# Optimization experiments

Measured on AMD Instinct MI355X. Metric: run time of the kernel, lower is better.

## Reference

```python
import jax, jax.numpy as jnp
import numpy as np

SCALE_VALUE = 1  # init kwarg; divide scores by sqrt(scale_value)


def setup_inputs() -> dict:
    key = jax.random.key(0)
    k1, k2 = jax.random.split(key)
    B, S, D = 8, 4096, 128
    inputs = jax.random.normal(k1, (B, S, D), dtype=jnp.float32)
    kernel = jax.random.normal(k2, (3, D, D), dtype=jnp.float32) * 0.05
    return {"inputs": inputs, "kernel": kernel}


def reference(inputs, kernel):
    # Q/K/V projections: [B,S,D] @ [D,D]
    wq = jnp.einsum('bsd,de->bse', inputs, kernel[0])
    wk = jnp.einsum('bsd,de->bse', inputs, kernel[1])
    wv = jnp.einsum('bsd,de->bse', inputs, kernel[2])
    # full attention score matrix [B,S,S], scaled by 1/sqrt(scale_value)
    qk = jnp.einsum('bqd,bkd->bqk', wq, wk) / (SCALE_VALUE ** 0.5)
    attn = jax.nn.softmax(qk, axis=-1)
    v = jnp.einsum('bqk,bkd->bqd', attn, wv)
    # mean pool over sequence -> [B,D]
    return jnp.mean(v, axis=1)
```

## Files before the change

kernel.cpp:

```cpp
#include <hip/hip_runtime.h>

#define Bsz 8
#define Ssz 4096
#define Dsz 128

typedef short bf16x8 __attribute__((ext_vector_type(8)));
typedef float f32x4 __attribute__((ext_vector_type(4)));
typedef float f32x16 __attribute__((ext_vector_type(16)));
typedef int i32x2 __attribute__((ext_vector_type(2)));
typedef int i32x4 __attribute__((ext_vector_type(4)));
typedef unsigned int u32;

union B8 { u32 u[4]; bf16x8 v; };

__device__ __forceinline__ u32 pkbf(float a, float b) {
  u32 ra = __float_as_uint(a) + 0x8000u;
  u32 rb = __float_as_uint(b) + 0x8000u;
  return __builtin_amdgcn_perm(rb, ra, 0x07060302u);
}
__device__ __forceinline__ short f2bf(float f) {
  u32 r = __float_as_uint(f) + 0x8000u;
  return (short)(r >> 16);
}

__device__ __forceinline__ void gll16(const void* g, void* l) {
  __builtin_amdgcn_global_load_lds((const __attribute__((address_space(1))) void*)g,
                                   (__attribute__((address_space(3))) void*)l, 16, 0, 0);
}


__global__ __launch_bounds__(256, 2) void proj_kernel(
    const float* __restrict__ x, const float* __restrict__ wsrc,
    short* __restrict__ Qs, short* __restrict__ Ks, short* __restrict__ Vp) {
  __shared__ short xb[64 * 136];
  __shared__ short ob[8192];

  const int rb = blockIdx.x;
  const int t = threadIdx.x;
  const int wv = t >> 6, lane = t & 63, l31 = lane & 31, h = lane >> 5;

  {
    const float* xsrc = x + (size_t)rb * 64 * Dsz;
    #pragma unroll
    for (int p = 0; p < 8; ++p) {
      int idx4 = p * 256 + t;
      int row = idx4 >> 5;
      int c4 = (idx4 & 31) << 2;
      f32x4 v = *(const f32x4*)&xsrc[idx4 * 4];
      i32x2 pr;
      pr[0] = pkbf(v[0], v[1]);
      pr[1] = pkbf(v[2], v[3]);
      *(i32x2*)&xb[row * 136 + c4] = pr;
    }
  }
  __syncthreads();

  bf16x8 xf[2][8];
  #pragma unroll
  for (int st = 0; st < 2; ++st)
    #pragma unroll
    for (int c = 0; c < 8; ++c)
      xf[st][c] = *(const bf16x8*)&xb[(st * 32 + l31) * 136 + c * 16 + 8 * h];

  for (int mat = 0; mat < 3; ++mat) {
    const float* wm = wsrc + (size_t)mat * Dsz * Dsz;
    const float scale = (mat == 0) ? 1.44269504088896340736f : 1.0f;
    bf16x8 wf[8];
    #pragma unroll
    for (int c = 0; c < 8; ++c) {
      const float* p = wm + (size_t)(c * 16 + 8 * h) * Dsz + wv * 32 + l31;
      B8 tmp;
      #pragma unroll
      for (int j = 0; j < 4; ++j)
        tmp.u[j] = pkbf(p[(2 * j) * Dsz] * scale, p[(2 * j + 1) * Dsz] * scale);
      wf[c] = tmp.v;
    }

    if (mat < 2) {
      #pragma unroll
      for (int st = 0; st < 2; ++st) {
        f32x16 acc = {};
        #pragma unroll
        for (int c = 0; c < 8; ++c)
          acc = __builtin_amdgcn_mfma_f32_32x32x16_bf16(wf[c], xf[st][c], acc, 0, 0, 0);
        if (st == 0) __syncthreads();
        #pragma unroll
        for (int g = 0; g < 4; ++g) {
          int e0 = wv * 32 + 8 * g + 4 * h;
          int s = st * 32 + l31;
          i32x2 pr;
          pr[0] = pkbf(acc[4 * g + 0], acc[4 * g + 1]);
          pr[1] = pkbf(acc[4 * g + 2], acc[4 * g + 3]);
          *(i32x2*)&ob[(e0 >> 3) * 512 + s * 8 + (e0 & 7)] = pr;
        }
      }
    } else {
      #pragma unroll
      for (int st = 0; st < 2; ++st) {
        f32x16 acc = {};
        #pragma unroll
        for (int c = 0; c < 8; ++c)
          acc = __builtin_amdgcn_mfma_f32_32x32x16_bf16(xf[st][c], wf[c], acc, 0, 0, 0);
        if (st == 0) __syncthreads();
        int e = wv * 32 + l31;
        #pragma unroll
        for (int r = 0; r < 16; ++r) {
          int s = st * 32 + (r & 3) + 8 * (r >> 2) + 4 * h;
          ob[s * 128 + e] = f2bf(acc[r]);
        }
      }
    }
    __syncthreads();
    short* dst = (mat == 0 ? Qs : mat == 1 ? Ks : Vp) + (size_t)rb * 8192;
    #pragma unroll
    for (int p = 0; p < 4; ++p)
      *(i32x4*)&dst[(p * 256 + t) * 8] = *(const i32x4*)&ob[(p * 256 + t) * 8];
  }
}

__global__ __launch_bounds__(256, 2) void lsum_kernel(
    const short* __restrict__ Qs, const short* __restrict__ Ks,
    float* __restrict__ lpart) {
  __shared__ short kbuf[2][16384];

  const int b = blockIdx.x, qt = blockIdx.y, kt = blockIdx.z;
  const int t = threadIdx.x;
  const int wv = t >> 6, lane = t & 63, l31 = lane & 31, h = lane >> 5;

  bf16x8 qf[2][8];
  {
    const short* qsrc = Qs + (size_t)(b * 64 + qt * 4 + wv) * 8192;
    #pragma unroll
    for (int nq = 0; nq < 2; ++nq)
      #pragma unroll
      for (int c = 0; c < 8; ++c)
        qf[nq][c] = *(const bf16x8*)&qsrc[(2 * c + h) * 512 + (nq * 32 + l31) * 8];
  }
  float rs2[2] = {0.f, 0.f};

  const char* kbase = (const char*)(Ks + (size_t)(b * 64 + kt * 16) * 8192);
  #define STAGE_K2(it_, bf_)                                                    \
    { const char* src_ = kbase + (size_t)(it_) * 32768;                         \
      _Pragma("unroll")                                                         \
      for (int i_ = 0; i_ < 8; ++i_) {                                          \
        int p_ = wv * 8 + i_;                                                   \
        gll16(src_ + p_ * 1024 + lane * 16, (char*)kbuf[bf_] + p_ * 1024);      \
      } }

  STAGE_K2(0, 0);
  __syncthreads();

  for (int it = 0; it < 8; ++it) {
    const int cur = it & 1;
    if (it < 7) STAGE_K2(it + 1, cur ^ 1);
    #pragma unroll
    for (int mk = 0; mk < 4; ++mk) {
      bf16x8 kf[8];
      #pragma unroll
      for (int c = 0; c < 8; ++c)
        kf[c] = *(const bf16x8*)&kbuf[cur][(mk >> 1) * 8192 + (2 * c + h) * 512 +
                                           ((mk & 1) * 32 + l31) * 8];
      f32x16 s0 = {}, s1 = {};
      #pragma unroll
      for (int c = 0; c < 8; ++c) {
        s0 = __builtin_amdgcn_mfma_f32_32x32x16_bf16(kf[c], qf[0][c], s0, 0, 0, 0);
        s1 = __builtin_amdgcn_mfma_f32_32x32x16_bf16(kf[c], qf[1][c], s1, 0, 0, 0);
      }
      #pragma unroll
      for (int r = 0; r < 16; ++r) rs2[0] += __builtin_amdgcn_exp2f(s0[r]);
      #pragma unroll
      for (int r = 0; r < 16; ++r) rs2[1] += __builtin_amdgcn_exp2f(s1[r]);
    }
    __syncthreads();
  }

  #pragma unroll
  for (int nq = 0; nq < 2; ++nq) {
    float v = rs2[nq] + __shfl_xor(rs2[nq], 32, 64);
    if (h == 0)
      lpart[((size_t)kt * 8 + b) * 4096 + qt * 256 + wv * 64 + nq * 32 + l31] = v;
  }
}

__global__ __launch_bounds__(256, 2) void attnv_kernel(
    const short* __restrict__ Qs, const short* __restrict__ Ks,
    const float* __restrict__ lpart, float* __restrict__ gpart) {
  __shared__ short kbuf[2][8192];
  __shared__ float linv_lds[256];
  __shared__ float gw[4][1024];

  const int b = blockIdx.x, qt = blockIdx.y, kt = blockIdx.z;
  const int t = threadIdx.x;
  const int wv = t >> 6, lane = t & 63, l31 = lane & 31, h = lane >> 5;

  {
    int q = qt * 256 + t;
    float l = 0.f;
    #pragma unroll
    for (int k2 = 0; k2 < 4; ++k2) l += lpart[((size_t)k2 * 8 + b) * 4096 + q];
    linv_lds[t] = 1.f / (l * (float)Ssz);
  }

  bf16x8 qf[2][8];
  {
    const short* qsrc = Qs + (size_t)(b * 64 + qt * 4 + wv) * 8192;
    #pragma unroll
    for (int mq = 0; mq < 2; ++mq)
      #pragma unroll
      for (int c = 0; c < 8; ++c)
        qf[mq][c] = *(const bf16x8*)&qsrc[(2 * c + h) * 512 + (mq * 32 + l31) * 8];
  }
  __syncthreads();

  float li[2][16];
  #pragma unroll
  for (int mq = 0; mq < 2; ++mq)
    #pragma unroll
    for (int r = 0; r < 16; ++r)
      li[mq][r] = linv_lds[wv * 64 + mq * 32 + (r & 3) + 8 * (r >> 2) + 4 * h];

  const char* kbase = (const char*)(Ks + (size_t)(b * 64 + kt * 16) * 8192);
  #define STAGE_K1(it_, bf_)                                                    \
    { const char* src_ = kbase + (size_t)(it_) * 16384;                         \
      _Pragma("unroll")                                                         \
      for (int i_ = 0; i_ < 4; ++i_) {                                          \
        int p_ = wv * 4 + i_;                                                   \
        gll16(src_ + p_ * 1024 + lane * 16, (char*)kbuf[bf_] + p_ * 1024);      \
      } }

  STAGE_K1(0, 0);
  __syncthreads();

  for (int it = 0; it < 16; ++it) {
    const int cur = it & 1;
    if (it < 15) STAGE_K1(it + 1, cur ^ 1);
    #pragma unroll
    for (int nk = 0; nk < 2; ++nk) {
      bf16x8 kf[8];
      #pragma unroll
      for (int c = 0; c < 8; ++c)
        kf[c] = *(const bf16x8*)&kbuf[cur][(2 * c + h) * 512 + (nk * 32 + l31) * 8];
      f32x16 s0 = {}, s1 = {};
      #pragma unroll
      for (int c = 0; c < 8; ++c) {
        s0 = __builtin_amdgcn_mfma_f32_32x32x16_bf16(qf[0][c], kf[c], s0, 0, 0, 0);
        s1 = __builtin_amdgcn_mfma_f32_32x32x16_bf16(qf[1][c], kf[c], s1, 0, 0, 0);
      }
      float gp = 0.f;
      #pragma unroll
      for (int r = 0; r < 16; ++r)
        gp += li[0][r] * __builtin_amdgcn_exp2f(s0[r]) +
              li[1][r] * __builtin_amdgcn_exp2f(s1[r]);
      gp += __shfl_xor(gp, 32, 64);
      if (h == 0) gw[wv][it * 64 + nk * 32 + l31] = gp;
    }
    __syncthreads();
  }

  float* gdst = gpart + (((size_t)(b * 16 + qt) * 4) + kt) * 1024;
  #pragma unroll
  for (int j = 0; j < 4; ++j) {
    int idx = j * 256 + t;
    gdst[idx] = (gw[0][idx] + gw[1][idx]) + (gw[2][idx] + gw[3][idx]);
  }
}

__global__ __launch_bounds__(256) void gemv_kernel(
    const float* __restrict__ gpart, const short* __restrict__ Vp,
    float* __restrict__ out) {
  __shared__ float Gs[128];
  __shared__ float pwb[512];
  const int b = blockIdx.x, ks = blockIdx.y;
  const int t = threadIdx.x;
  if (t < 128) {
    int k = ks * 128 + t;
    int kt = k >> 10, kl = k & 1023;
    float s = 0.f;
    #pragma unroll
    for (int qt = 0; qt < 16; ++qt)
      s += gpart[(((size_t)(b * 16 + qt) * 4) + kt) * 1024 + kl];
    Gs[t] = s;
  }
  __syncthreads();
  const int dp = t & 63, kq = t >> 6;
  const short* vr = Vp + ((size_t)b * 4096 + ks * 128 + kq * 32) * 128 + 2 * dp;
  float a0 = 0.f, a1 = 0.f;
  #pragma unroll 8
  for (int k = 0; k < 32; ++k) {
    u32 pair = *(const u32*)&vr[(size_t)k * 128];
    float g = Gs[kq * 32 + k];
    a0 += g * __uint_as_float(pair << 16);
    a1 += g * __uint_as_float(pair & 0xffff0000u);
  }
  pwb[kq * 128 + 2 * dp] = a0;
  pwb[kq * 128 + 2 * dp + 1] = a1;
  __syncthreads();
  if (t < 128) {
    float s = (pwb[t] + pwb[128 + t]) + (pwb[256 + t] + pwb[384 + t]);
    atomicAdd(&out[b * 128 + t], s);
  }
}

extern "C" void kernel_launch(void* const* d_in, const int* in_sizes, int n_in,
                              void* d_out, int out_size, void* d_ws, size_t ws_size,
                              hipStream_t stream) {
  const float* x = (const float*)d_in[0];
  const float* w = (const float*)d_in[1];
  short* Qs = (short*)d_ws;
  short* Ks = Qs + (size_t)Bsz * Ssz * Dsz;
  short* Vp = Ks + (size_t)Bsz * Ssz * Dsz;
  float* lpart = (float*)(Vp + (size_t)Bsz * Ssz * Dsz);
  float* gpart = lpart + 4 * Bsz * Ssz;

  hipMemsetAsync(d_out, 0, Bsz * Dsz * sizeof(float), stream);
  proj_kernel<<<dim3(Bsz * Ssz / 64), dim3(256), 0, stream>>>(x, w, Qs, Ks, Vp);
  lsum_kernel<<<dim3(Bsz, 16, 4), dim3(256), 0, stream>>>(Qs, Ks, lpart);
  attnv_kernel<<<dim3(Bsz, 16, 4), dim3(256), 0, stream>>>(Qs, Ks, lpart, gpart);
  gemv_kernel<<<dim3(Bsz, 32), dim3(256), 0, stream>>>(gpart, Vp, (float*)d_out);
}
```

Baseline: 144.3 us.

## Widen attention blocks to 512 threads, fold normalization into MFMA accumulator, drop memset

```diff
diff --git a/kernel.cpp b/kernel.cpp
--- a/kernel.cpp
+++ b/kernel.cpp
@@ -31,13 +31,16 @@
 
 __global__ __launch_bounds__(256, 2) void proj_kernel(
     const float* __restrict__ x, const float* __restrict__ wsrc,
-    short* __restrict__ Qs, short* __restrict__ Ks, short* __restrict__ Vp) {
+    short* __restrict__ Qs, short* __restrict__ Ks, short* __restrict__ Vp,
+    float* __restrict__ out0) {
   __shared__ short xb[64 * 136];
   __shared__ short ob[8192];
 
   const int rb = blockIdx.x;
   const int t = threadIdx.x;
   const int wv = t >> 6, lane = t & 63, l31 = lane & 31, h = lane >> 5;
+
+  if (rb < 4) out0[rb * 256 + t] = 0.f;
 
   {
     const float* xsrc = x + (size_t)rb * 64 * Dsz;
@@ -118,7 +121,7 @@
   }
 }
 
-__global__ __launch_bounds__(256, 2) void lsum_kernel(
+__global__ __launch_bounds__(512, 4) void lsum_kernel(
     const short* __restrict__ Qs, const short* __restrict__ Ks,
     float* __restrict__ lpart) {
   __shared__ short kbuf[2][16384];
@@ -129,7 +132,7 @@
 
   bf16x8 qf[2][8];
   {
-    const short* qsrc = Qs + (size_t)(b * 64 + qt * 4 + wv) * 8192;
+    const short* qsrc = Qs + (size_t)(b * 64 + qt * 8 + wv) * 8192;
     #pragma unroll
     for (int nq = 0; nq < 2; ++nq)
       #pragma unroll
@@ -138,131 +141,120 @@
   }
   float rs2[2] = {0.f, 0.f};
 
-  const char* kbase = (const char*)(Ks + (size_t)(b * 64 + kt * 16) * 8192);
-  #define STAGE_K2(it_, bf_)                                                    \
+  const char* kbase = (const char*)(Ks + (size_t)(b * 64 + kt * 8) * 8192);
+  #define STAGE2(it_, bf_)                                                      \
     { const char* src_ = kbase + (size_t)(it_) * 32768;                         \
-      _Pragma("unroll")                                                         \
-      for (int i_ = 0; i_ < 8; ++i_) {                                          \
-        int p_ = wv * 8 + i_;                                                   \
-        gll16(src_ + p_ * 1024 + lane * 16, (char*)kbuf[bf_] + p_ * 1024);      \
-      } }
-
-  STAGE_K2(0, 0);
-  __syncthreads();
-
-  for (int it = 0; it < 8; ++it) {
-    const int cur = it & 1;
-    if (it < 7) STAGE_K2(it + 1, cur ^ 1);
-    #pragma unroll
-    for (int mk = 0; mk < 4; ++mk) {
-      bf16x8 kf[8];
-      #pragma unroll
-      for (int c = 0; c < 8; ++c)
-        kf[c] = *(const bf16x8*)&kbuf[cur][(mk >> 1) * 8192 + (2 * c + h) * 512 +
-                                           ((mk & 1) * 32 + l31) * 8];
-      f32x16 s0 = {}, s1 = {};
-      #pragma unroll
-      for (int c = 0; c < 8; ++c) {
-        s0 = __builtin_amdgcn_mfma_f32_32x32x16_bf16(kf[c], qf[0][c], s0, 0, 0, 0);
-        s1 = __builtin_amdgcn_mfma_f32_32x32x16_bf16(kf[c], qf[1][c], s1, 0, 0, 0);
-      }
-      #pragma unroll
-      for (int r = 0; r < 16; ++r) rs2[0] += __builtin_amdgcn_exp2f(s0[r]);
-      #pragma unroll
-      for (int r = 0; r < 16; ++r) rs2[1] += __builtin_amdgcn_exp2f(s1[r]);
-    }
-    __syncthreads();
-  }
-
-  #pragma unroll
-  for (int nq = 0; nq < 2; ++nq) {
-    float v = rs2[nq] + __shfl_xor(rs2[nq], 32, 64);
-    if (h == 0)
-      lpart[((size_t)kt * 8 + b) * 4096 + qt * 256 + wv * 64 + nq * 32 + l31] = v;
-  }
-}
-
-__global__ __launch_bounds__(256, 2) void attnv_kernel(
-    const short* __restrict__ Qs, const short* __restrict__ Ks,
-    const float* __restrict__ lpart, float* __restrict__ gpart) {
-  __shared__ short kbuf[2][8192];
-  __shared__ float linv_lds[256];
-  __shared__ float gw[4][1024];
-
-  const int b = blockIdx.x, qt = blockIdx.y, kt = blockIdx.z;
-  const int t = threadIdx.x;
-  const int wv = t >> 6, lane = t & 63, l31 = lane & 31, h = lane >> 5;
-
-  {
-    int q = qt * 256 + t;
-    float l = 0.f;
-    #pragma unroll
-    for (int k2 = 0; k2 < 4; ++k2) l += lpart[((size_t)k2 * 8 + b) * 4096 + q];
-    linv_lds[t] = 1.f / (l * (float)Ssz);
-  }
-
-  bf16x8 qf[2][8];
-  {
-    const short* qsrc = Qs + (size_t)(b * 64 + qt * 4 + wv) * 8192;
-    #pragma unroll
-    for (int mq = 0; mq < 2; ++mq)
-      #pragma unroll
-      for (int c = 0; c < 8; ++c)
-        qf[mq][c] = *(const bf16x8*)&qsrc[(2 * c + h) * 512 + (mq * 32 + l31) * 8];
-  }
-  __syncthreads();
-
-  float li[2][16];
-  #pragma unroll
-  for (int mq = 0; mq < 2; ++mq)
-    #pragma unroll
-    for (int r = 0; r < 16; ++r)
-      li[mq][r] = linv_lds[wv * 64 + mq * 32 + (r & 3) + 8 * (r >> 2) + 4 * h];
-
-  const char* kbase = (const char*)(Ks + (size_t)(b * 64 + kt * 16) * 8192);
-  #define STAGE_K1(it_, bf_)                                                    \
-    { const char* src_ = kbase + (size_t)(it_) * 16384;                         \
       _Pragma("unroll")                                                         \
       for (int i_ = 0; i_ < 4; ++i_) {                                          \
         int p_ = wv * 4 + i_;                                                   \
         gll16(src_ + p_ * 1024 + lane * 16, (char*)kbuf[bf_] + p_ * 1024);      \
       } }
 
-  STAGE_K1(0, 0);
-  __syncthreads();
-
-  for (int it = 0; it < 16; ++it) {
+  STAGE2(0, 0);
+  __syncthreads();
+
+  for (int it = 0; it < 4; ++it) {
     const int cur = it & 1;
-    if (it < 15) STAGE_K1(it + 1, cur ^ 1);
+    if (it < 3) STAGE2(it + 1, cur ^ 1);
+    #pragma unroll
+    for (int mk = 0; mk < 4; ++mk) {
+      const int kb0 = (mk >> 1) * 8192 + ((mk & 1) * 32 + l31) * 8;
+      f32x16 s0 = {}, s1 = {};
+      #pragma unroll
+      for (int c = 0; c < 8; ++c) {
+        bf16x8 kf = *(const bf16x8*)&kbuf[cur][kb0 + (2 * c + h) * 512];
+        s0 = __builtin_amdgcn_mfma_f32_32x32x16_bf16(kf, qf[0][c], s0, 0, 0, 0);
+        s1 = __builtin_amdgcn_mfma_f32_32x32x16_bf16(kf, qf[1][c], s1, 0, 0, 0);
+      }
+      #pragma unroll
+      for (int r = 0; r < 16; ++r) rs2[0] += __builtin_amdgcn_exp2f(s0[r]);
+      #pragma unroll
+      for (int r = 0; r < 16; ++r) rs2[1] += __builtin_amdgcn_exp2f(s1[r]);
+    }
+    __syncthreads();
+  }
+
+  #pragma unroll
+  for (int nq = 0; nq < 2; ++nq) {
+    float v = rs2[nq] + __shfl_xor(rs2[nq], 32, 64);
+    if (h == 0)
+      lpart[((size_t)kt * 8 + b) * 4096 + qt * 512 + wv * 64 + nq * 32 + l31] = v;
+  }
+}
+
+__global__ __launch_bounds__(512, 4) void attnv_kernel(
+    const short* __restrict__ Qs, const short* __restrict__ Ks,
+    const float* __restrict__ lpart, float* __restrict__ gpart) {
+  __shared__ short kbuf[2][8192];
+  __shared__ float ladj_lds[512];
+  __shared__ float gw[8][512];
+
+  const int b = blockIdx.x, qt = blockIdx.y, kt = blockIdx.z;
+  const int t = threadIdx.x;
+  const int wv = t >> 6, lane = t & 63, l31 = lane & 31, h = lane >> 5;
+
+  {
+    int q = qt * 512 + t;
+    float l = 0.f;
+    #pragma unroll
+    for (int k2 = 0; k2 < 8; ++k2) l += lpart[((size_t)k2 * 8 + b) * 4096 + q];
+    ladj_lds[t] = -(__builtin_amdgcn_logf(l) + 12.0f);
+  }
+
+  bf16x8 qf[2][8];
+  {
+    const short* qsrc = Qs + (size_t)(b * 64 + qt * 8 + wv) * 8192;
+    #pragma unroll
+    for (int mq = 0; mq < 2; ++mq)
+      #pragma unroll
+      for (int c = 0; c < 8; ++c)
+        qf[mq][c] = *(const bf16x8*)&qsrc[(2 * c + h) * 512 + (mq * 32 + l31) * 8];
+  }
+  __syncthreads();
+
+  const char* kbase = (const char*)(Ks + (size_t)(b * 64 + kt * 8) * 8192);
+  #define STAGE1(it_, bf_)                                                      \
+    { const char* src_ = kbase + (size_t)(it_) * 16384;                         \
+      _Pragma("unroll")                                                         \
+      for (int i_ = 0; i_ < 2; ++i_) {                                          \
+        int p_ = wv * 2 + i_;                                                   \
+        gll16(src_ + p_ * 1024 + lane * 16, (char*)kbuf[bf_] + p_ * 1024);      \
+      } }
+
+  STAGE1(0, 0);
+  __syncthreads();
+
+  for (int it = 0; it < 8; ++it) {
+    const int cur = it & 1;
+    if (it < 7) STAGE1(it + 1, cur ^ 1);
     #pragma unroll
     for (int nk = 0; nk < 2; ++nk) {
-      bf16x8 kf[8];
-      #pragma unroll
-      for (int c = 0; c < 8; ++c)
-        kf[c] = *(const bf16x8*)&kbuf[cur][(2 * c + h) * 512 + (nk * 32 + l31) * 8];
-      f32x16 s0 = {}, s1 = {};
-      #pragma unroll
-      for (int c = 0; c < 8; ++c) {
-        s0 = __builtin_amdgcn_mfma_f32_32x32x16_bf16(qf[0][c], kf[c], s0, 0, 0, 0);
-        s1 = __builtin_amdgcn_mfma_f32_32x32x16_bf16(qf[1][c], kf[c], s1, 0, 0, 0);
+      const int kb0 = (nk * 32 + l31) * 8;
+      float gp = 0.f;
+      #pragma unroll
+      for (int nq = 0; nq < 2; ++nq) {
+        f32x16 sc;
+        #pragma unroll
+        for (int r = 0; r < 16; ++r)
+          sc[r] = ladj_lds[wv * 64 + nq * 32 + (r & 3) + 8 * (r >> 2) + 4 * h];
+        #pragma unroll
+        for (int c = 0; c < 8; ++c) {
+          bf16x8 kf = *(const bf16x8*)&kbuf[cur][kb0 + (2 * c + h) * 512];
+          sc = __builtin_amdgcn_mfma_f32_32x32x16_bf16(qf[nq][c], kf, sc, 0, 0, 0);
+        }
+        #pragma unroll
+        for (int r = 0; r < 16; ++r) gp += __builtin_amdgcn_exp2f(sc[r]);
       }
-      float gp = 0.f;
-      #pragma unroll
-      for (int r = 0; r < 16; ++r)
-        gp += li[0][r] * __builtin_amdgcn_exp2f(s0[r]) +
-              li[1][r] * __builtin_amdgcn_exp2f(s1[r]);
       gp += __shfl_xor(gp, 32, 64);
       if (h == 0) gw[wv][it * 64 + nk * 32 + l31] = gp;
     }
     __syncthreads();
   }
 
-  float* gdst = gpart + (((size_t)(b * 16 + qt) * 4) + kt) * 1024;
+  float s = 0.f;
   #pragma unroll
-  for (int j = 0; j < 4; ++j) {
-    int idx = j * 256 + t;
-    gdst[idx] = (gw[0][idx] + gw[1][idx]) + (gw[2][idx] + gw[3][idx]);
-  }
+  for (int w2 = 0; w2 < 8; ++w2) s += gw[w2][t];
+  gpart[(((size_t)(b * 8 + qt) * 8) + kt) * 512 + t] = s;
 }
 
 __global__ __launch_bounds__(256) void gemv_kernel(
@@ -274,11 +266,11 @@
   const int t = threadIdx.x;
   if (t < 128) {
     int k = ks * 128 + t;
-    int kt = k >> 10, kl = k & 1023;
+    int kt = k >> 9, kl = k & 511;
     float s = 0.f;
     #pragma unroll
-    for (int qt = 0; qt < 16; ++qt)
-      s += gpart[(((size_t)(b * 16 + qt) * 4) + kt) * 1024 + kl];
+    for (int qt = 0; qt < 8; ++qt)
+      s += gpart[(((size_t)(b * 8 + qt) * 8) + kt) * 512 + kl];
     Gs[t] = s;
   }
   __syncthreads();
@@ -310,11 +302,11 @@
   short* Ks = Qs + (size_t)Bsz * Ssz * Dsz;
   short* Vp = Ks + (size_t)Bsz * Ssz * Dsz;
   float* lpart = (float*)(Vp + (size_t)Bsz * Ssz * Dsz);
-  float* gpart = lpart + 4 * Bsz * Ssz;
-
-  hipMemsetAsync(d_out, 0, Bsz * Dsz * sizeof(float), stream);
-  proj_kernel<<<dim3(Bsz * Ssz / 64), dim3(256), 0, stream>>>(x, w, Qs, Ks, Vp);
-  lsum_kernel<<<dim3(Bsz, 16, 4), dim3(256), 0, stream>>>(Qs, Ks, lpart);
-  attnv_kernel<<<dim3(Bsz, 16, 4), dim3(256), 0, stream>>>(Qs, Ks, lpart, gpart);
+  float* gpart = lpart + 8 * Bsz * Ssz;
+
+  proj_kernel<<<dim3(Bsz * Ssz / 64), dim3(256), 0, stream>>>(x, w, Qs, Ks, Vp,
+                                                              (float*)d_out);
+  lsum_kernel<<<dim3(Bsz, 8, 8), dim3(512), 0, stream>>>(Qs, Ks, lpart);
+  attnv_kernel<<<dim3(Bsz, 8, 8), dim3(512), 0, stream>>>(Qs, Ks, lpart, gpart);
   gemv_kernel<<<dim3(Bsz, 32), dim3(256), 0, stream>>>(gpart, Vp, (float*)d_out);
 }
```

Result: slower. 215.4 us (+49.2%).
